# Optimization experiments

Hardware: AMD Instinct MI355X
Metric: run time of the kernel (lower is better)

Reference implementation:

```python
import jax, jax.numpy as jnp
import numpy as np

B, D, NT, NZ = 16384, 64, 128, 2048


def setup_inputs() -> dict:
    key = jax.random.key(0)
    ks = jax.random.split(key, 5)
    return {
        "t": jax.random.uniform(ks[0], (1,), dtype=jnp.float32),
        "z": jax.random.normal(ks[1], (B, D), dtype=jnp.float32),
        "logp_z": jnp.zeros((B, 1), jnp.float32),
        "centres_z": jax.random.normal(ks[2], (NZ, D), dtype=jnp.float32),
        "log_sigmas_z": jnp.zeros((NZ,), jnp.float32),
        "centres_t": jax.random.normal(ks[3], (NT, 1), dtype=jnp.float32),
        "log_sigmas_t": jnp.zeros((NT,), jnp.float32),
        "W": 0.01 * jax.random.normal(ks[4], (D, NT, NZ + 1), dtype=jnp.float32),
    }


def _gauss(r):
    return jnp.exp(-r * r)


def _forward(t, z, centres_z, log_sigmas_z, centres_t, log_sigmas_t, W):
    # time RBF features Phi_t: (NT,)
    r_t = jnp.abs(t.reshape(1, 1) - centres_t.reshape(1, -1)) / jnp.exp(log_sigmas_t)
    phi_t = _gauss(r_t).reshape(-1)
    W_t = jnp.einsum('dij,i->dj', W, phi_t)  # (D, NZ+1)
    Wz, bias = W_t[:, :-1], W_t[:, -1]       # bias comes from the appended ones column
    # z RBF features via squared-distance identity (avoids [B,NZ,D] blowup)
    sq = (jnp.sum(z * z, axis=1, keepdims=True)
          + jnp.sum(centres_z * centres_z, axis=1)[None, :]
          - 2.0 * z @ centres_z.T)
    sq = jnp.maximum(sq, 0.0)                 # (B, NZ) squared distances
    inv_s2 = jnp.exp(-2.0 * log_sigmas_z)     # 1/sigma_j^2, (NZ,)
    phi_z = jnp.exp(-sq * inv_s2)             # gaussian(||z-c_j||/s_j), (B, NZ)
    dz_dt = phi_z @ Wz.T + bias               # (B, D)
    # exact Jacobian trace for gaussian basis:
    #   d phi_j / d z_i = -2 * phi_j * (z_i - c_{j,i}) / s_j^2
    #   tr(J)_b = sum_j phi_{b,j} * inv_s2_j * (-2) * (sum_i Wz[i,j] z_{b,i} - sum_i Wz[i,j] c_{j,i})
    q = jnp.einsum('dj,jd->j', Wz, centres_z)  # (NZ,)
    trace = -2.0 * jnp.sum(phi_z * inv_s2 * (z @ Wz - q), axis=1)  # (B,)
    dlogp_z_dt = -trace[:, None]               # (B, 1)
    return dz_dt, dlogp_z_dt


def reference(t, z, logp_z, centres_z, log_sigmas_z, centres_t, log_sigmas_t, W):
    return _forward(t, z, centres_z, log_sigmas_z, centres_t, log_sigmas_t, W)
```

## Files before the change

### kernel.cpp

```cpp
#include <hip/hip_runtime.h>
#include <math.h>

typedef unsigned int uint;
typedef unsigned short ushort;
typedef unsigned char uchar;
typedef unsigned long ulong_;
typedef __attribute__((ext_vector_type(4))) float f32x4;

#define BB  16384
#define DD  64
#define NT_ 128
#define NZ_ 2048
#define NJ_ 2049

#define BIAS_OFF 0
#define SCS_OFF  64
#define CZ8A_OFF 8256
#define CZ8B_OFF 24640
#define WZ8A_OFF 41024
#define WZ8B_OFF 57408
#define WZBP_OFF 73792
#define PART_OFF 106560

#if __has_builtin(__builtin_amdgcn_cvt_pk_fp8_f32)
__device__ __forceinline__ uint pk4_fp8(float a, float b, float c, float d) {
  int v = __builtin_amdgcn_cvt_pk_fp8_f32(a, b, 0, false);
  v = __builtin_amdgcn_cvt_pk_fp8_f32(c, d, v, true);
  return (uint)v;
}
__device__ __forceinline__ uchar f8_1(float x) {
  return (uchar)(__builtin_amdgcn_cvt_pk_fp8_f32(x, x, 0, false) & 0xFF);
}
#else
__device__ __forceinline__ uint sw_f8(float x) {
  uint u = __float_as_uint(x);
  uint s = (u >> 24) & 0x80u;
  float ax = __uint_as_float(u & 0x7FFFFFFFu);
  if (!(ax >= 0.015625f)) return s;
  if (ax >= 448.f) return s | 0x7Eu;
  uint q = __float_as_uint(ax);
  q += 0x7FFFFu + ((q >> 20) & 1u);
  uint e = (q >> 23) - 120u;
  return s | ((e & 0xFu) << 3) | ((q >> 20) & 7u);
}
__device__ __forceinline__ uchar f8_1(float x) { return (uchar)sw_f8(x); }
__device__ __forceinline__ uint pk4_fp8(float a, float b, float c, float d) {
  return sw_f8(a) | (sw_f8(b) << 8) | (sw_f8(c) << 16) | (sw_f8(d) << 24);
}
#endif

__global__ __launch_bounds__(256) void k_wt1(
    const float* __restrict__ t, const float* __restrict__ ct,
    const float* __restrict__ lst, const float* __restrict__ W,
    float* __restrict__ part)
{
  __shared__ float ph[32];
  int tx = threadIdx.x;
  int d  = blockIdx.y;
  int ic = blockIdx.z;
  if (tx < 32) {
    int i = ic * 32 + tx;
    float r = fabsf(t[0] - ct[i]) * __expf(-lst[i]);
    ph[tx] = __expf(-r * r);
  }
  __syncthreads();
  int j = blockIdx.x * 256 + tx;
  if (j >= NJ_) return;
  const float* Wp = W + (size_t)d * NT_ * NJ_ + (size_t)(ic * 32) * NJ_ + j;
  float acc = 0.f;
#pragma unroll
  for (int k = 0; k < 32; ++k) acc += Wp[(size_t)k * NJ_] * ph[k];
  part[((size_t)ic * 64 + d) * NJ_ + j] = acc;
}

__global__ __launch_bounds__(256) void k_prep2(
    const float* __restrict__ part, const float* __restrict__ cz,
    const float* __restrict__ lsz,
    float* __restrict__ bias, float4* __restrict__ scs,
    uchar* __restrict__ cz8a, uchar* __restrict__ cz8b,
    uchar* __restrict__ wz8a, uchar* __restrict__ wz8b,
    uchar* __restrict__ wzbp8)
{
  __shared__ float wt[64][9];
  int tid = threadIdx.x;
  int cb0 = blockIdx.x * 8;
#pragma unroll
  for (int h = 0; h < 2; ++h) {
    int f = h * 256 + tid;
    int d = f >> 3, c = f & 7;
    size_t idx = (size_t)d * NJ_ + cb0 + c;
    float s = part[idx] + part[(size_t)64 * NJ_ + idx]
            + part[(size_t)128 * NJ_ + idx] + part[(size_t)192 * NJ_ + idx];
    wt[d][c] = s;
    int cg = cb0 + c;
    wzbp8[((size_t)(cg >> 5) * 64 + d) * 32 + (cg & 31)] = f8_1(s);
  }
  if (blockIdx.x == 0 && tid < 64) {
    size_t idx = (size_t)tid * NJ_ + 2048;
    bias[tid] = part[idx] + part[(size_t)64 * NJ_ + idx]
              + part[(size_t)128 * NJ_ + idx] + part[(size_t)192 * NJ_ + idx];
  }
  __syncthreads();
  int cl = tid >> 5;
  int k  = tid & 31;
  int c  = cb0 + cl;
  float cv0 = cz[(size_t)c * DD + k];
  float cv1 = cz[(size_t)c * DD + 32 + k];
  cz8a[(size_t)c * 32 + k] = f8_1(cv0);
  cz8b[(size_t)c * 32 + k] = f8_1(cv1);
  float w0 = wt[k][cl], w1 = wt[32 + k][cl];
  wz8a[(size_t)c * 32 + k] = f8_1(w0);
  wz8b[(size_t)c * 32 + k] = f8_1(w1);
  float ca = cv0 * cv0 + cv1 * cv1;
  float qa = w0 * cv0 + w1 * cv1;
  qa += __shfl_xor(qa, 1);  ca += __shfl_xor(ca, 1);
  qa += __shfl_xor(qa, 2);  ca += __shfl_xor(ca, 2);
  qa += __shfl_xor(qa, 4);  ca += __shfl_xor(ca, 4);
  qa += __shfl_xor(qa, 8);  ca += __shfl_xor(ca, 8);
  qa += __shfl_xor(qa, 16); ca += __shfl_xor(ca, 16);
  if (k == 0) {
    float inv = __expf(-2.f * lsz[c]);
    scs[c] = make_float4(ca, inv, qa, inv * 1.44269504f);
  }
}

#define PH_LD 40

__global__ __launch_bounds__(256) void k_fused(
    const float* __restrict__ z,
    const uchar* __restrict__ cz8a, const uchar* __restrict__ cz8b,
    const uchar* __restrict__ wz8a, const uchar* __restrict__ wz8b,
    const uchar* __restrict__ wzbp8,
    const float4* __restrict__ scs, const float* __restrict__ bias,
    float* __restrict__ out)
{
  __shared__ char smem[10240];
  __shared__ float dlr[4][32];
  uchar* phs = (uchar*)smem;
  float* eps = (float*)smem;

  int tid  = threadIdx.x;
  int ws   = tid >> 6;
  int lane = tid & 63;
  int lrow = lane & 15, quad = lane >> 4;
  int b0 = blockIdx.x * 32;

  long az[2][2];
  float zzr[2][4];
#pragma unroll
  for (int mt = 0; mt < 2; ++mt) {
    const float* zr = z + (size_t)(b0 + mt * 16 + lrow) * DD + quad * 8;
    float4 v0 = *(const float4*)zr;
    float4 v1 = *(const float4*)(zr + 4);
    float4 v2 = *(const float4*)(zr + 32);
    float4 v3 = *(const float4*)(zr + 36);
    uint l0 = pk4_fp8(v0.x, v0.y, v0.z, v0.w);
    uint l1 = pk4_fp8(v1.x, v1.y, v1.z, v1.w);
    uint h0 = pk4_fp8(v2.x, v2.y, v2.z, v2.w);
    uint h1 = pk4_fp8(v3.x, v3.y, v3.z, v3.w);
    az[mt][0] = (long)(((ulong_)l1 << 32) | l0);
    az[mt][1] = (long)(((ulong_)h1 << 32) | h0);
    float ss = v0.x * v0.x + v0.y * v0.y + v0.z * v0.z + v0.w * v0.w
             + v1.x * v1.x + v1.y * v1.y + v1.z * v1.z + v1.w * v1.w
             + v2.x * v2.x + v2.y * v2.y + v2.z * v2.z + v2.w * v2.w
             + v3.x * v3.x + v3.y * v3.y + v3.z * v3.z + v3.w * v3.w;
    ss += __shfl_xor(ss, 16);
    ss += __shfl_xor(ss, 32);
#pragma unroll
    for (int i = 0; i < 4; ++i) zzr[mt][i] = __shfl(ss, quad * 4 + i);
  }

  f32x4 acc[2][4];
#pragma unroll
  for (int mt = 0; mt < 2; ++mt)
#pragma unroll
    for (int nt = 0; nt < 4; ++nt) acc[mt][nt] = (f32x4){0.f, 0.f, 0.f, 0.f};
  float dl[2][4] = {{0.f}};

  const f32x4 zero = (f32x4){0.f, 0.f, 0.f, 0.f};
  int cbase = ws * 512;
  int pbase = ws * 32 * PH_LD;

  long Abc0[2][2], Abc1[2][2], Abw0[2][2], Abw1[2][2], Abb[2][4];
  float4 Asc[2][2];
#define LOADB(PAR, C0)                                                         \
  do {                                                                         \
    int c0_ = (C0);                                                            \
    _Pragma("unroll")                                                          \
    for (int nt = 0; nt < 2; ++nt) {                                           \
      int cg_ = c0_ + nt * 16 + lrow;                                          \
      size_t ro_ = (size_t)cg_ * 32 + quad * 8;                                \
      Abc0[PAR][nt] = *(const long*)(cz8a + ro_);                              \
      Abc1[PAR][nt] = *(const long*)(cz8b + ro_);                              \
      Abw0[PAR][nt] = *(const long*)(wz8a + ro_);                              \
      Abw1[PAR][nt] = *(const long*)(wz8b + ro_);                              \
      Asc[PAR][nt]  = scs[cg_];                                                \
    }                                                                          \
    size_t cb_ = (size_t)(c0_ >> 5) * 64 * 32;                                 \
    _Pragma("unroll")                                                          \
    for (int nt = 0; nt < 4; ++nt)                                             \
      Abb[PAR][nt] =                                                           \
          *(const long*)(wzbp8 + cb_ + (size_t)(nt * 16 + lrow) * 32 + quad * 8); \
  } while (0)

  LOADB(0, cbase);
#pragma unroll 2
  for (int it = 0; it < 16; ++it) {
    int par = it & 1;
    LOADB(par ^ 1, cbase + ((it + 1) & 15) * 32);

    int pb = par * (4 * 32 * PH_LD) + pbase;
#pragma unroll
    for (int nt = 0; nt < 2; ++nt) {
      float4 sc = Asc[par][nt];
#pragma unroll
      for (int mt = 0; mt < 2; ++mt) {
        f32x4 d1 = __builtin_amdgcn_mfma_f32_16x16x32_fp8_fp8(az[mt][0], Abc0[par][nt], zero, 0, 0, 0);
        d1       = __builtin_amdgcn_mfma_f32_16x16x32_fp8_fp8(az[mt][1], Abc1[par][nt], d1,   0, 0, 0);
        f32x4 d2 = __builtin_amdgcn_mfma_f32_16x16x32_fp8_fp8(az[mt][0], Abw0[par][nt], zero, 0, 0, 0);
        d2       = __builtin_amdgcn_mfma_f32_16x16x32_fp8_fp8(az[mt][1], Abw1[par][nt], d2,   0, 0, 0);
#pragma unroll
        for (int i = 0; i < 4; ++i) {
          float e = fmaf(d1[i], 2.f, -(zzr[mt][i] + sc.x)) * sc.w;
          e = fminf(e, 0.f);
          float p;
          asm("v_exp_f32 %0, %1" : "=v"(p) : "v"(e));
          dl[mt][i] += p * sc.y * (d2[i] - sc.z);
          phs[pb + (mt * 16 + quad * 4 + i) * PH_LD + nt * 16 + lrow] = f8_1(p);
        }
      }
    }
    long ap0 = *(const long*)&phs[pb + lrow * PH_LD + quad * 8];
    long ap1 = *(const long*)&phs[pb + (16 + lrow) * PH_LD + quad * 8];
    __builtin_amdgcn_s_setprio(1);
#pragma unroll
    for (int nt = 0; nt < 4; ++nt) {
      acc[0][nt] = __builtin_amdgcn_mfma_f32_16x16x32_fp8_fp8(ap0, Abb[par][nt], acc[0][nt], 0, 0, 0);
      acc[1][nt] = __builtin_amdgcn_mfma_f32_16x16x32_fp8_fp8(ap1, Abb[par][nt], acc[1][nt], 0, 0, 0);
    }
    __builtin_amdgcn_s_setprio(0);
  }
#undef LOADB

#pragma unroll
  for (int mt = 0; mt < 2; ++mt)
#pragma unroll
    for (int i = 0; i < 4; ++i) {
      float v = dl[mt][i];
      v += __shfl_xor(v, 1);
      v += __shfl_xor(v, 2);
      v += __shfl_xor(v, 4);
      v += __shfl_xor(v, 8);
      if (lrow == 0) dlr[ws][mt * 16 + quad * 4 + i] = v;
    }

  for (int s = 0; s < 4; ++s) {
    __syncthreads();
    if (ws == s) {
#pragma unroll
      for (int mt = 0; mt < 2; ++mt)
#pragma unroll
        for (int nt = 0; nt < 4; ++nt)
#pragma unroll
          for (int i = 0; i < 4; ++i) {
            int r = mt * 16 + quad * 4 + i;
            int d = nt * 16 + lrow;
            if (s == 0) eps[r * 68 + d] = acc[mt][nt][i];
            else        eps[r * 68 + d] += acc[mt][nt][i];
          }
    }
  }
  __syncthreads();

  {
    int r = tid >> 3, d0 = (tid & 7) * 8;
    float4 e0 = *(const float4*)&eps[r * 68 + d0];
    float4 e1 = *(const float4*)&eps[r * 68 + d0 + 4];
    float4 bv0 = *(const float4*)&bias[d0];
    float4 bv1 = *(const float4*)&bias[d0 + 4];
    float4 o0, o1;
    o0.x = e0.x + bv0.x; o0.y = e0.y + bv0.y; o0.z = e0.z + bv0.z; o0.w = e0.w + bv0.w;
    o1.x = e1.x + bv1.x; o1.y = e1.y + bv1.y; o1.z = e1.z + bv1.z; o1.w = e1.w + bv1.w;
    *(float4*)&out[(size_t)(b0 + r) * DD + d0]     = o0;
    *(float4*)&out[(size_t)(b0 + r) * DD + d0 + 4] = o1;
  }
  if (tid < 32) {
    float s = dlr[0][tid] + dlr[1][tid] + dlr[2][tid] + dlr[3][tid];
    out[(size_t)BB * DD + b0 + tid] = 2.f * s;
  }
}

extern "C" void kernel_launch(void* const* d_in, const int* in_sizes, int n_in,
                              void* d_out, int out_size, void* d_ws, size_t ws_size,
                              hipStream_t stream)
{
  const float* t   = (const float*)d_in[0];
  const float* z   = (const float*)d_in[1];
  const float* cz  = (const float*)d_in[3];
  const float* lsz = (const float*)d_in[4];
  const float* ct  = (const float*)d_in[5];
  const float* lst = (const float*)d_in[6];
  const float* W   = (const float*)d_in[7];
  float* out = (float*)d_out;
  float* ws  = (float*)d_ws;

  float*  bias = ws + BIAS_OFF;
  float4* scs  = (float4*)(ws + SCS_OFF);
  uchar*  cz8a = (uchar*)(ws + CZ8A_OFF);
  uchar*  cz8b = (uchar*)(ws + CZ8B_OFF);
  uchar*  wz8a = (uchar*)(ws + WZ8A_OFF);
  uchar*  wz8b = (uchar*)(ws + WZ8B_OFF);
  uchar*  wzbp8 = (uchar*)(ws + WZBP_OFF);
  float*  part = ws + PART_OFF;

  k_wt1<<<dim3(9, 64, 4), 256, 0, stream>>>(t, ct, lst, W, part);
  k_prep2<<<dim3(256), 256, 0, stream>>>(part, cz, lsz, bias, scs,
                                         cz8a, cz8b, wz8a, wz8b, wzbp8);
  k_fused<<<dim3(BB / 32), 256, 0, stream>>>(z, cz8a, cz8b,
                                             wz8a, wz8b, wzbp8, scs, bias, out);
}
```

Measured before the change: 138.7 us.

## Fuse three kernels into one persistent kernel with grid-wide atomic barriers

Merges the W-time contraction, the prep/quantization step and the main fused RBF kernel into a single 512-block launch. Blocks first compute their slice of W_t, the fp8 weights, the centres and the bias, then synchronise through two atomic-counter grid barriers before the MFMA phase. This removes two kernel launches and the partial-sum buffer round trip, at the cost of spin-wait barriers. The barriers only avoid deadlock if all 512 blocks are co-resident, which the code relies on through launch bounds (256, 2). It also adds a memset launch to reset the flags.

```diff
diff --git a/kernel.cpp b/kernel.cpp
--- a/kernel.cpp
+++ b/kernel.cpp
@@ -13,14 +13,15 @@
 #define NZ_ 2048
 #define NJ_ 2049
 
-#define BIAS_OFF 0
-#define SCS_OFF  64
-#define CZ8A_OFF 8256
-#define CZ8B_OFF 24640
-#define WZ8A_OFF 41024
-#define WZ8B_OFF 57408
-#define WZBP_OFF 73792
-#define PART_OFF 106560
+#define FLAG_OFF 0
+#define BIAS_OFF 16
+#define SCS_OFF  80
+#define CZ8A_OFF 8272
+#define CZ8B_OFF 24656
+#define WZ8A_OFF 41040
+#define WZ8B_OFF 57424
+#define WZBP_OFF 73808
+#define WT_OFF   106576
 
 #if __has_builtin(__builtin_amdgcn_cvt_pk_fp8_f32)
 __device__ __forceinline__ uint pk4_fp8(float a, float b, float c, float d) {
@@ -49,101 +50,33 @@
 }
 #endif
 
-__global__ __launch_bounds__(256) void k_wt1(
-    const float* __restrict__ t, const float* __restrict__ ct,
-    const float* __restrict__ lst, const float* __restrict__ W,
-    float* __restrict__ part)
-{
-  __shared__ float ph[32];
-  int tx = threadIdx.x;
-  int d  = blockIdx.y;
-  int ic = blockIdx.z;
-  if (tx < 32) {
-    int i = ic * 32 + tx;
-    float r = fabsf(t[0] - ct[i]) * __expf(-lst[i]);
-    ph[tx] = __expf(-r * r);
-  }
-  __syncthreads();
-  int j = blockIdx.x * 256 + tx;
-  if (j >= NJ_) return;
-  const float* Wp = W + (size_t)d * NT_ * NJ_ + (size_t)(ic * 32) * NJ_ + j;
-  float acc = 0.f;
-#pragma unroll
-  for (int k = 0; k < 32; ++k) acc += Wp[(size_t)k * NJ_] * ph[k];
-  part[((size_t)ic * 64 + d) * NJ_ + j] = acc;
-}
-
-__global__ __launch_bounds__(256) void k_prep2(
-    const float* __restrict__ part, const float* __restrict__ cz,
-    const float* __restrict__ lsz,
-    float* __restrict__ bias, float4* __restrict__ scs,
+#define PH_LD 40
+
+__global__ __launch_bounds__(256, 2) void k_all(
+    const float* __restrict__ t, const float* __restrict__ z,
+    const float* __restrict__ cz, const float* __restrict__ lsz,
+    const float* __restrict__ ct, const float* __restrict__ lst,
+    const float* __restrict__ W,
+    uint* __restrict__ flags, float* __restrict__ bias,
+    float4* __restrict__ scs,
     uchar* __restrict__ cz8a, uchar* __restrict__ cz8b,
     uchar* __restrict__ wz8a, uchar* __restrict__ wz8b,
-    uchar* __restrict__ wzbp8)
-{
-  __shared__ float wt[64][9];
-  int tid = threadIdx.x;
-  int cb0 = blockIdx.x * 8;
-#pragma unroll
-  for (int h = 0; h < 2; ++h) {
-    int f = h * 256 + tid;
-    int d = f >> 3, c = f & 7;
-    size_t idx = (size_t)d * NJ_ + cb0 + c;
-    float s = part[idx] + part[(size_t)64 * NJ_ + idx]
-            + part[(size_t)128 * NJ_ + idx] + part[(size_t)192 * NJ_ + idx];
-    wt[d][c] = s;
-    int cg = cb0 + c;
-    wzbp8[((size_t)(cg >> 5) * 64 + d) * 32 + (cg & 31)] = f8_1(s);
-  }
-  if (blockIdx.x == 0 && tid < 64) {
-    size_t idx = (size_t)tid * NJ_ + 2048;
-    bias[tid] = part[idx] + part[(size_t)64 * NJ_ + idx]
-              + part[(size_t)128 * NJ_ + idx] + part[(size_t)192 * NJ_ + idx];
-  }
-  __syncthreads();
-  int cl = tid >> 5;
-  int k  = tid & 31;
-  int c  = cb0 + cl;
-  float cv0 = cz[(size_t)c * DD + k];
-  float cv1 = cz[(size_t)c * DD + 32 + k];
-  cz8a[(size_t)c * 32 + k] = f8_1(cv0);
-  cz8b[(size_t)c * 32 + k] = f8_1(cv1);
-  float w0 = wt[k][cl], w1 = wt[32 + k][cl];
-  wz8a[(size_t)c * 32 + k] = f8_1(w0);
-  wz8b[(size_t)c * 32 + k] = f8_1(w1);
-  float ca = cv0 * cv0 + cv1 * cv1;
-  float qa = w0 * cv0 + w1 * cv1;
-  qa += __shfl_xor(qa, 1);  ca += __shfl_xor(ca, 1);
-  qa += __shfl_xor(qa, 2);  ca += __shfl_xor(ca, 2);
-  qa += __shfl_xor(qa, 4);  ca += __shfl_xor(ca, 4);
-  qa += __shfl_xor(qa, 8);  ca += __shfl_xor(ca, 8);
-  qa += __shfl_xor(qa, 16); ca += __shfl_xor(ca, 16);
-  if (k == 0) {
-    float inv = __expf(-2.f * lsz[c]);
-    scs[c] = make_float4(ca, inv, qa, inv * 1.44269504f);
-  }
-}
-
-#define PH_LD 40
-
-__global__ __launch_bounds__(256) void k_fused(
-    const float* __restrict__ z,
-    const uchar* __restrict__ cz8a, const uchar* __restrict__ cz8b,
-    const uchar* __restrict__ wz8a, const uchar* __restrict__ wz8b,
-    const uchar* __restrict__ wzbp8,
-    const float4* __restrict__ scs, const float* __restrict__ bias,
+    uchar* __restrict__ wzbp8, float* __restrict__ wt32,
     float* __restrict__ out)
 {
   __shared__ char smem[10240];
   __shared__ float dlr[4][32];
+  __shared__ float phi_t[NT_];
+  __shared__ float bred[2];
   uchar* phs = (uchar*)smem;
   float* eps = (float*)smem;
 
   int tid  = threadIdx.x;
-  int ws   = tid >> 6;
+  int bid  = blockIdx.x;
+  int wsp  = tid >> 6;
   int lane = tid & 63;
   int lrow = lane & 15, quad = lane >> 4;
-  int b0 = blockIdx.x * 32;
+  int b0 = bid * 32;
 
   long az[2][2];
   float zzr[2][4];
@@ -170,6 +103,87 @@
     for (int i = 0; i < 4; ++i) zzr[mt][i] = __shfl(ss, quad * 4 + i);
   }
 
+  int dA = bid >> 3, jblk = bid & 7;
+  if (tid < NT_) {
+    float r = fabsf(t[0] - ct[tid]) * __expf(-lst[tid]);
+    phi_t[tid] = __expf(-r * r);
+  }
+  __syncthreads();
+  {
+    int j = jblk * 256 + tid;
+    const float* Wp = W + (size_t)dA * NT_ * NJ_ + j;
+    float acc = 0.f;
+#pragma unroll 16
+    for (int k = 0; k < NT_; ++k) acc += Wp[(size_t)k * NJ_] * phi_t[k];
+    wt32[(size_t)dA * NJ_ + j] = acc;
+    uchar a8 = f8_1(acc);
+    wzbp8[(size_t)(j >> 5) * 2048 + dA * 32 + (j & 31)] = a8;
+    if (dA < 32) wz8a[(size_t)j * 32 + dA] = a8;
+    else         wz8b[(size_t)j * 32 + (dA - 32)] = a8;
+  }
+  {
+    float bv = 0.f;
+    if (jblk == 0 && tid < NT_)
+      bv = W[(size_t)dA * NT_ * NJ_ + (size_t)tid * NJ_ + 2048] * phi_t[tid];
+    bv += __shfl_xor(bv, 1);
+    bv += __shfl_xor(bv, 2);
+    bv += __shfl_xor(bv, 4);
+    bv += __shfl_xor(bv, 8);
+    bv += __shfl_xor(bv, 16);
+    bv += __shfl_xor(bv, 32);
+    if (jblk == 0 && tid < NT_ && lane == 0) bred[tid >> 6] = bv;
+  }
+  {
+    int c = bid * 4 + wsp;
+    float v = cz[(size_t)c * DD + lane];
+    uchar c8 = f8_1(v);
+    if (lane < 32) cz8a[(size_t)c * 32 + lane] = c8;
+    else           cz8b[(size_t)c * 32 + (lane - 32)] = c8;
+    float ss = v * v;
+    ss += __shfl_xor(ss, 1);
+    ss += __shfl_xor(ss, 2);
+    ss += __shfl_xor(ss, 4);
+    ss += __shfl_xor(ss, 8);
+    ss += __shfl_xor(ss, 16);
+    ss += __shfl_xor(ss, 32);
+    if (lane == 0) {
+      float inv = __expf(-2.f * lsz[c]);
+      scs[c] = make_float4(ss, inv, 0.f, inv * 1.44269504f);
+    }
+  }
+  __syncthreads();
+  if (jblk == 0 && tid == 0) bias[dA] = bred[0] + bred[1];
+
+  __threadfence();
+  if (tid == 0) {
+    atomicAdd(&flags[0], 1u);
+    while (__hip_atomic_load(&flags[0], __ATOMIC_ACQUIRE,
+                             __HIP_MEMORY_SCOPE_AGENT) < 512u)
+      __builtin_amdgcn_s_sleep(2);
+  }
+  __syncthreads();
+
+  {
+    int c = bid * 4 + wsp;
+    float qv = wt32[(size_t)lane * NJ_ + c] * cz[(size_t)c * DD + lane];
+    qv += __shfl_xor(qv, 1);
+    qv += __shfl_xor(qv, 2);
+    qv += __shfl_xor(qv, 4);
+    qv += __shfl_xor(qv, 8);
+    qv += __shfl_xor(qv, 16);
+    qv += __shfl_xor(qv, 32);
+    if (lane == 0) ((float*)&scs[c])[2] = qv;
+  }
+
+  __threadfence();
+  if (tid == 0) {
+    atomicAdd(&flags[1], 1u);
+    while (__hip_atomic_load(&flags[1], __ATOMIC_ACQUIRE,
+                             __HIP_MEMORY_SCOPE_AGENT) < 512u)
+      __builtin_amdgcn_s_sleep(2);
+  }
+  __syncthreads();
+
   f32x4 acc[2][4];
 #pragma unroll
   for (int mt = 0; mt < 2; ++mt)
@@ -178,8 +192,8 @@
   float dl[2][4] = {{0.f}};
 
   const f32x4 zero = (f32x4){0.f, 0.f, 0.f, 0.f};
-  int cbase = ws * 512;
-  int pbase = ws * 32 * PH_LD;
+  int cbase = wsp * 512;
+  int pbase = wsp * 32 * PH_LD;
 
   long Abc0[2][2], Abc1[2][2], Abw0[2][2], Abw1[2][2], Abb[2][4];
   float4 Asc[2][2];
@@ -251,12 +265,12 @@
       v += __shfl_xor(v, 2);
       v += __shfl_xor(v, 4);
       v += __shfl_xor(v, 8);
-      if (lrow == 0) dlr[ws][mt * 16 + quad * 4 + i] = v;
+      if (lrow == 0) dlr[wsp][mt * 16 + quad * 4 + i] = v;
     }
 
   for (int s = 0; s < 4; ++s) {
     __syncthreads();
-    if (ws == s) {
+    if (wsp == s) {
 #pragma unroll
       for (int mt = 0; mt < 2; ++mt)
 #pragma unroll
@@ -264,9 +278,9 @@
 #pragma unroll
           for (int i = 0; i < 4; ++i) {
             int r = mt * 16 + quad * 4 + i;
-            int d = nt * 16 + lrow;
-            if (s == 0) eps[r * 68 + d] = acc[mt][nt][i];
-            else        eps[r * 68 + d] += acc[mt][nt][i];
+            int dd = nt * 16 + lrow;
+            if (s == 0) eps[r * 68 + dd] = acc[mt][nt][i];
+            else        eps[r * 68 + dd] += acc[mt][nt][i];
           }
     }
   }
@@ -304,18 +318,18 @@
   float* out = (float*)d_out;
   float* ws  = (float*)d_ws;
 
-  float*  bias = ws + BIAS_OFF;
-  float4* scs  = (float4*)(ws + SCS_OFF);
-  uchar*  cz8a = (uchar*)(ws + CZ8A_OFF);
-  uchar*  cz8b = (uchar*)(ws + CZ8B_OFF);
-  uchar*  wz8a = (uchar*)(ws + WZ8A_OFF);
-  uchar*  wz8b = (uchar*)(ws + WZ8B_OFF);
+  uint*   flags = (uint*)(ws + FLAG_OFF);
+  float*  bias  = ws + BIAS_OFF;
+  float4* scs   = (float4*)(ws + SCS_OFF);
+  uchar*  cz8a  = (uchar*)(ws + CZ8A_OFF);
+  uchar*  cz8b  = (uchar*)(ws + CZ8B_OFF);
+  uchar*  wz8a  = (uchar*)(ws + WZ8A_OFF);
+  uchar*  wz8b  = (uchar*)(ws + WZ8B_OFF);
   uchar*  wzbp8 = (uchar*)(ws + WZBP_OFF);
-  float*  part = ws + PART_OFF;
-
-  k_wt1<<<dim3(9, 64, 4), 256, 0, stream>>>(t, ct, lst, W, part);
-  k_prep2<<<dim3(256), 256, 0, stream>>>(part, cz, lsz, bias, scs,
-                                         cz8a, cz8b, wz8a, wz8b, wzbp8);
-  k_fused<<<dim3(BB / 32), 256, 0, stream>>>(z, cz8a, cz8b,
-                                             wz8a, wz8b, wzbp8, scs, bias, out);
-}
+  float*  wt32  = ws + WT_OFF;
+
+  hipMemsetAsync((void*)flags, 0, 16, stream);
+  k_all<<<dim3(512), 256, 0, stream>>>(t, z, cz, lsz, ct, lst, W,
+                                       flags, bias, scs,
+                                       cz8a, cz8b, wz8a, wz8b, wzbp8, wt32, out);
+}
```

Result: slower. 288.0 us (+107.7%).
